# Kernel optimization log

Measured on AMD Instinct MI355X. Metric: run time of the kernel, lower is better.

The kernel has to match this reference:

```python
import jax, jax.numpy as jnp
import numpy as np

DG = 4      # deformable groups
PAD = 1     # (kernel_size - 1) // 2
KH = KW = 3


def deform_conv(x, offset, weight, dg=DG, pad=PAD):
    """DCN v1 (mmcv layout): offset channels = dg * 2 * K, per group ordered
    (y0, x0, y1, x1, ...) over kernel points in row-major order.
    x: [B, C, H, W]; offset: [B, dg*2*K, H, W]; weight: [Cout, C, kh, kw].
    """
    B, C, H, W = x.shape
    Cout, Cin, kh, kw = weight.shape
    K = kh * kw
    Cg = C // dg
    off = offset.reshape(B, dg, K, 2, H, W)

    ys = jnp.arange(H, dtype=x.dtype)
    xs = jnp.arange(W, dtype=x.dtype)
    kyy = jnp.repeat(jnp.arange(kh, dtype=x.dtype) - pad, kw)   # [K]
    kxx = jnp.tile(jnp.arange(kw, dtype=x.dtype) - pad, kh)     # [K]

    # fractional sampling positions, [B, dg, K, H, W]
    py = ys[None, :, None] + kyy[:, None, None] + off[:, :, :, 0]
    px = xs[None, None, :] + kxx[:, None, None] + off[:, :, :, 1]

    y0 = jnp.floor(py)
    x0 = jnp.floor(px)
    ty = py - y0
    tx = px - x0
    y1 = y0 + 1.0
    x1 = x0 + 1.0

    x_flat = x.reshape(B, dg, Cg, H * W)
    acc = jnp.zeros((B, dg, Cg, K, H, W), dtype=x.dtype)
    corners = [
        (y0, x0, (1.0 - ty) * (1.0 - tx)),
        (y0, x1, (1.0 - ty) * tx),
        (y1, x0, ty * (1.0 - tx)),
        (y1, x1, ty * tx),
    ]
    for yc, xc, wgt in corners:
        valid = (yc >= 0) & (yc <= H - 1) & (xc >= 0) & (xc <= W - 1)
        yi = jnp.clip(yc, 0, H - 1).astype(jnp.int32)
        xi = jnp.clip(xc, 0, W - 1).astype(jnp.int32)
        idx = (yi * W + xi).reshape(B, dg, 1, K * H * W)
        v = jnp.take_along_axis(x_flat, idx, axis=3).reshape(B, dg, Cg, K, H, W)
        wv = jnp.where(valid, wgt, 0.0)[:, :, None]  # [B, dg, 1, K, H, W]
        acc = acc + v * wv

    w = weight.reshape(Cout, dg, Cg, kh * kw)
    return jnp.einsum('bgckhw,ogck->bohw', acc, w)


def setup_inputs() -> dict:
    key = jax.random.key(0)
    ks = jax.random.split(key, 6)
    B, C, H, W = 8, 256, 64, 64
    return {
        'reg_feat': jax.random.normal(ks[0], (B, C, H, W), jnp.float32),
        'cls_feat': jax.random.normal(ks[1], (B, C, H, W), jnp.float32),
        'pred_init': jax.random.normal(ks[2], (B, 34, H, W), jnp.float32),
        'w_offset': jax.random.normal(ks[3], (DG * 2 * KH * KW, 34), jnp.float32) * 0.1,
        'w_reg': jax.random.normal(ks[4], (C, C, KH, KW), jnp.float32) * 0.01,
        'w_cls': jax.random.normal(ks[5], (C, C, KH, KW), jnp.float32) * 0.01,
    }


def reference(reg_feat, cls_feat, pred_init, w_offset, w_reg, w_cls):
    # 1x1 offset conv on detached anchor-shape prediction
    offset = jnp.einsum('bchw,oc->bohw', jax.lax.stop_gradient(pred_init), w_offset)
    reg_refine = jax.nn.relu(deform_conv(reg_feat, offset, w_reg))
    cls_refine = jax.nn.relu(deform_conv(cls_feat, offset, w_cls))
    return (reg_refine, cls_refine)
```

## Files before the change

### kernel.cpp

```cpp
#include <hip/hip_runtime.h>

#define B_   8
#define C_   256
#define HW_  4096
#define OC_  72
#define PC_  34
#define CLS_OFF (B_ * C_ * HW_)

typedef __attribute__((ext_vector_type(8))) short short8v;
typedef __attribute__((ext_vector_type(4))) float f32x4;

__device__ __forceinline__ ushort f2bf(float f) {
  uint u = __float_as_uint(f);
  return (ushort)((u + 0x7fffu + ((u >> 16) & 1u)) >> 16);
}
__device__ __forceinline__ float bf2f(ushort h) {
  return __uint_as_float(((uint)h) << 16);
}

__global__ __launch_bounds__(256)
void offset_kernel(const float* __restrict__ pred, const float* __restrict__ wo,
                   float* __restrict__ offset) {
  const int p  = blockIdx.x * 256 + threadIdx.x;
  const int b  = p >> 12;
  const int hw = p & 4095;
  const float* pp = pred + (size_t)b * PC_ * HW_ + hw;
  float v[PC_];
#pragma unroll
  for (int i = 0; i < PC_; ++i) v[i] = pp[(size_t)i * HW_];
  float* op = offset + (size_t)b * OC_ * HW_ + hw;
  for (int o = 0; o < OC_; ++o) {
    float s = 0.f;
#pragma unroll
    for (int i = 0; i < PC_; ++i) s = fmaf(v[i], wo[o * PC_ + i], s);
    op[(size_t)o * HW_] = s;
  }
}

__global__ __launch_bounds__(256)
void repack_w(const float* __restrict__ w_reg, const float* __restrict__ w_cls,
              ushort* __restrict__ wpk) {
  const int tid = blockIdx.x * 256 + threadIdx.x;
  const int l   = tid & 63;
  const int mf  = (tid >> 6) & 15;
  int rest = tid >> 10;
  const int kk  = rest & 1; rest >>= 1;
  const int s   = rest % 36;
  const int map = rest / 36;
  const float* src = map ? w_cls : w_reg;
  const int g = s / 9, kp = s % 9;
  const int o = mf * 16 + (l & 15);
  const int cbase = kk * 32 + (l >> 4) * 8;
  union { ushort u[8]; short8v v; } hu, lu;
#pragma unroll
  for (int j = 0; j < 8; ++j) {
    const int c = cbase + j;
    const float v = src[o * 2304 + (g * 64 + c) * 9 + kp];
    const ushort h = f2bf(v);
    hu.u[j] = h;
    lu.u[j] = f2bf(v - bf2f(h));
  }
  const size_t eb = ((size_t)((map * 36 + s) * 2 + kk)) * 16384 + mf * 512 + l * 8;
  *reinterpret_cast<short8v*>(wpk + eb)        = hu.v;
  *reinterpret_cast<short8v*>(wpk + eb + 8192) = lu.v;
}

__device__ __forceinline__ void calc_params(const float* __restrict__ off, int b,
                                            int px0, int t, int ss,
                                            int (*sIdx)[64][4], float (*sWt)[64][4],
                                            int bb) {
  const int hw = px0 + t;
  const int y = hw >> 6, x = hw & 63;
  const int kp = ss % 9;
  const float oy = off[((size_t)b * OC_ + 2 * ss) * HW_ + hw];
  const float ox = off[((size_t)b * OC_ + 2 * ss + 1) * HW_ + hw];
  const float py  = (float)(y + kp / 3 - 1) + oy;
  const float pxx = (float)(x + kp % 3 - 1) + ox;
  const float y0f = floorf(py), x0f = floorf(pxx);
  const float ty = py - y0f, tx = pxx - x0f;
  const int y0 = (int)y0f, x0 = (int)x0f;
  const int y1 = y0 + 1, x1 = x0 + 1;
  const bool vy0 = (y0 >= 0) & (y0 <= 63), vy1 = (y1 >= 0) & (y1 <= 63);
  const bool vx0 = (x0 >= 0) & (x0 <= 63), vx1 = (x1 >= 0) & (x1 <= 63);
  const int cy0 = min(max(y0, 0), 63), cy1 = min(max(y1, 0), 63);
  const int cx0 = min(max(x0, 0), 63), cx1 = min(max(x1, 0), 63);
  sIdx[bb][t][0] = cy0 * 64 + cx0; sWt[bb][t][0] = (vy0 && vx0) ? (1.f - ty) * (1.f - tx) : 0.f;
  sIdx[bb][t][1] = cy0 * 64 + cx1; sWt[bb][t][1] = (vy0 && vx1) ? (1.f - ty) * tx : 0.f;
  sIdx[bb][t][2] = cy1 * 64 + cx0; sWt[bb][t][2] = (vy1 && vx0) ? ty * (1.f - tx) : 0.f;
  sIdx[bb][t][3] = cy1 * 64 + cx1; sWt[bb][t][3] = (vy1 && vx1) ? ty * tx : 0.f;
}

__global__ __launch_bounds__(256)
void deform_mfma(const float* __restrict__ xreg, const float* __restrict__ xcls,
                 const float* __restrict__ off, const ushort* __restrict__ wpk,
                 float* __restrict__ out) {
  __shared__ ushort Bh[4096];
  __shared__ ushort Bl[4096];
  __shared__ int   sIdx[2][64][4];
  __shared__ float sWt[2][64][4];

  const int lin = blockIdx.y * 512 + blockIdx.x;
  const int nid = (lin & 7) * 128 + (lin >> 3);
  const int map = nid >> 9;
  const int nt  = nid & 511;
  const int b   = nt >> 6;
  const int px0 = (nt & 63) * 64;

  const int t = threadIdx.x;
  const int lane = t & 63, wid = t >> 6;
  const float* xsrc = map ? xcls : xreg;

  f32x4 acc[4][4];
#pragma unroll
  for (int mf = 0; mf < 4; ++mf)
#pragma unroll
    for (int nf = 0; nf < 4; ++nf) acc[mf][nf] = (f32x4){0.f, 0.f, 0.f, 0.f};

  if (t < 64) calc_params(off, b, px0, t, 0, sIdx, sWt, 0);
  __syncthreads();

  for (int s = 0; s < 36; ++s) {
    const int pb = s & 1;
    const int g  = s / 9;

    short8v a_h[2][4], a_l[2][4];
    const size_t abase = ((size_t)(map * 36 + s)) * 32768 + lane * 8;
#pragma unroll
    for (int kk = 0; kk < 2; ++kk)
#pragma unroll
      for (int mf = 0; mf < 4; ++mf) {
        const size_t e = abase + (size_t)kk * 16384 + (wid * 4 + mf) * 512;
        a_h[kk][mf] = *reinterpret_cast<const short8v*>(wpk + e);
        a_l[kk][mf] = *reinterpret_cast<const short8v*>(wpk + e + 8192);
      }

    {
      const int px  = t & 63;
      const int kgb = t >> 6;
      const int i0 = sIdx[pb][px][0], i1 = sIdx[pb][px][1],
                i2 = sIdx[pb][px][2], i3 = sIdx[pb][px][3];
      const float w0 = sWt[pb][px][0], w1 = sWt[pb][px][1],
                  w2 = sWt[pb][px][2], w3 = sWt[pb][px][3];
#pragma unroll
      for (int q = 0; q < 2; ++q) {
        const int kg = kgb + q * 4;
        const float* xb = xsrc + ((size_t)((b * 4 + g) * 64 + kg * 8)) * HW_;
        union { ushort u[8]; short8v v; } hu, lu;
#pragma unroll
        for (int i = 0; i < 8; ++i) {
          const float* xc = xb + (size_t)i * HW_;
          const float v = w0 * xc[i0] + w1 * xc[i1] + w2 * xc[i2] + w3 * xc[i3];
          const ushort h = f2bf(v);
          hu.u[i] = h;
          lu.u[i] = f2bf(v - bf2f(h));
        }
        const int slot = ((kg >> 2) * 4 + (px >> 4)) * 64 + ((kg & 3) * 16 + (px & 15));
        *reinterpret_cast<short8v*>(Bh + slot * 8) = hu.v;
        *reinterpret_cast<short8v*>(Bl + slot * 8) = lu.v;
      }
    }

    if (s + 1 < 36 && t < 64) calc_params(off, b, px0, t, s + 1, sIdx, sWt, pb ^ 1);
    __syncthreads();

#pragma unroll
    for (int kk = 0; kk < 2; ++kk) {
      short8v bh[4], bl[4];
#pragma unroll
      for (int nf = 0; nf < 4; ++nf) {
        bh[nf] = *reinterpret_cast<const short8v*>(Bh + ((kk * 4 + nf) * 64 + lane) * 8);
        bl[nf] = *reinterpret_cast<const short8v*>(Bl + ((kk * 4 + nf) * 64 + lane) * 8);
      }
#pragma unroll
      for (int mf = 0; mf < 4; ++mf)
#pragma unroll
        for (int nf = 0; nf < 4; ++nf) {
          f32x4 c = acc[mf][nf];
          c = __builtin_amdgcn_mfma_f32_16x16x32_bf16(a_l[kk][mf], bh[nf], c, 0, 0, 0);
          c = __builtin_amdgcn_mfma_f32_16x16x32_bf16(a_h[kk][mf], bl[nf], c, 0, 0, 0);
          c = __builtin_amdgcn_mfma_f32_16x16x32_bf16(a_h[kk][mf], bh[nf], c, 0, 0, 0);
          acc[mf][nf] = c;
        }
    }
    __syncthreads();
  }

  float* obase = out + (map ? CLS_OFF : 0) + (size_t)b * C_ * HW_ + px0;
  const int m0 = wid * 64;
#pragma unroll
  for (int mf = 0; mf < 4; ++mf)
#pragma unroll
    for (int nf = 0; nf < 4; ++nf)
#pragma unroll
      for (int r = 0; r < 4; ++r) {
        const int o = m0 + mf * 16 + (lane >> 4) * 4 + r;
        const int n = nf * 16 + (lane & 15);
        obase[(size_t)o * HW_ + n] = fmaxf(acc[mf][nf][r], 0.f);
      }
}

extern "C" void kernel_launch(void* const* d_in, const int* in_sizes, int n_in,
                              void* d_out, int out_size, void* d_ws, size_t ws_size,
                              hipStream_t stream) {
  const float* reg_feat = (const float*)d_in[0];
  const float* cls_feat = (const float*)d_in[1];
  const float* pred     = (const float*)d_in[2];
  const float* w_off    = (const float*)d_in[3];
  const float* w_reg    = (const float*)d_in[4];
  const float* w_cls    = (const float*)d_in[5];
  float* outp = (float*)d_out;

  float*  offset = (float*)d_ws;
  ushort* wpk    = (ushort*)((char*)d_ws + (size_t)B_ * OC_ * HW_ * 4);

  offset_kernel<<<dim3((B_ * HW_) / 256), 256, 0, stream>>>(pred, w_off, offset);
  repack_w<<<dim3(576), 256, 0, stream>>>(w_reg, w_cls, wpk);
  deform_mfma<<<dim3(512, 2), dim3(256), 0, stream>>>(reg_feat, cls_feat,
                                                      offset, wpk, outp);
}
```

Before: 637.5 us.

## Software-pipeline deformable gather with MFMA using double-buffered LDS and merged prep kernel

The main kernel now double-buffers the bf16 hi/lo B tiles in LDS. It issues the global gathers for step s+1 into registers before running the MFMAs for step s, then converts and stores them afterwards, so gather latency overlaps with matrix math and one barrier per step is removed. Bilinear parameters are computed per thread in registers from prefetched offsets instead of being staged through shared memory. The offset and weight-repack kernels are merged into one launch, and launch bounds, s_setprio and a changed LDS slot mapping are added. The cost is higher register pressure (64 gathered floats per thread), which may limit occupancy.

```diff
diff --git a/kernel.cpp b/kernel.cpp
--- a/kernel.cpp
+++ b/kernel.cpp
@@ -19,63 +19,57 @@
 }
 
 __global__ __launch_bounds__(256)
-void offset_kernel(const float* __restrict__ pred, const float* __restrict__ wo,
-                   float* __restrict__ offset) {
-  const int p  = blockIdx.x * 256 + threadIdx.x;
-  const int b  = p >> 12;
-  const int hw = p & 4095;
-  const float* pp = pred + (size_t)b * PC_ * HW_ + hw;
-  float v[PC_];
-#pragma unroll
-  for (int i = 0; i < PC_; ++i) v[i] = pp[(size_t)i * HW_];
-  float* op = offset + (size_t)b * OC_ * HW_ + hw;
-  for (int o = 0; o < OC_; ++o) {
-    float s = 0.f;
-#pragma unroll
-    for (int i = 0; i < PC_; ++i) s = fmaf(v[i], wo[o * PC_ + i], s);
-    op[(size_t)o * HW_] = s;
+void prep_kernel(const float* __restrict__ pred, const float* __restrict__ wo,
+                 const float* __restrict__ w_reg, const float* __restrict__ w_cls,
+                 float* __restrict__ offset, ushort* __restrict__ wpk) {
+  if (blockIdx.x < 128) {
+    const int p  = blockIdx.x * 256 + threadIdx.x;
+    const int b  = p >> 12;
+    const int hw = p & 4095;
+    const float* pp = pred + (size_t)b * PC_ * HW_ + hw;
+    float v[PC_];
+#pragma unroll
+    for (int i = 0; i < PC_; ++i) v[i] = pp[(size_t)i * HW_];
+    float* op = offset + (size_t)b * OC_ * HW_ + hw;
+    for (int o = 0; o < OC_; ++o) {
+      float s = 0.f;
+#pragma unroll
+      for (int i = 0; i < PC_; ++i) s = fmaf(v[i], wo[o * PC_ + i], s);
+      op[(size_t)o * HW_] = s;
+    }
+  } else {
+    const int tid = (blockIdx.x - 128) * 256 + threadIdx.x;
+    const int l   = tid & 63;
+    const int mf  = (tid >> 6) & 15;
+    int rest = tid >> 10;
+    const int kk  = rest & 1; rest >>= 1;
+    const int s   = rest % 36;
+    const int map = rest / 36;
+    const float* src = map ? w_cls : w_reg;
+    const int g = s / 9, kp = s % 9;
+    const int o = mf * 16 + (l & 15);
+    const int cbase = kk * 32 + (l >> 4) * 8;
+    union { ushort u[8]; short8v v; } hu, lu;
+#pragma unroll
+    for (int j = 0; j < 8; ++j) {
+      const int c = cbase + j;
+      const float v = src[o * 2304 + (g * 64 + c) * 9 + kp];
+      const ushort h = f2bf(v);
+      hu.u[j] = h;
+      lu.u[j] = f2bf(v - bf2f(h));
+    }
+    const size_t eb = ((size_t)((map * 36 + s) * 2 + kk)) * 16384 + mf * 512 + l * 8;
+    *reinterpret_cast<short8v*>(wpk + eb)        = hu.v;
+    *reinterpret_cast<short8v*>(wpk + eb + 8192) = lu.v;
   }
 }
 
-__global__ __launch_bounds__(256)
-void repack_w(const float* __restrict__ w_reg, const float* __restrict__ w_cls,
-              ushort* __restrict__ wpk) {
-  const int tid = blockIdx.x * 256 + threadIdx.x;
-  const int l   = tid & 63;
-  const int mf  = (tid >> 6) & 15;
-  int rest = tid >> 10;
-  const int kk  = rest & 1; rest >>= 1;
-  const int s   = rest % 36;
-  const int map = rest / 36;
-  const float* src = map ? w_cls : w_reg;
-  const int g = s / 9, kp = s % 9;
-  const int o = mf * 16 + (l & 15);
-  const int cbase = kk * 32 + (l >> 4) * 8;
-  union { ushort u[8]; short8v v; } hu, lu;
-#pragma unroll
-  for (int j = 0; j < 8; ++j) {
-    const int c = cbase + j;
-    const float v = src[o * 2304 + (g * 64 + c) * 9 + kp];
-    const ushort h = f2bf(v);
-    hu.u[j] = h;
-    lu.u[j] = f2bf(v - bf2f(h));
-  }
-  const size_t eb = ((size_t)((map * 36 + s) * 2 + kk)) * 16384 + mf * 512 + l * 8;
-  *reinterpret_cast<short8v*>(wpk + eb)        = hu.v;
-  *reinterpret_cast<short8v*>(wpk + eb + 8192) = lu.v;
-}
-
-__device__ __forceinline__ void calc_params(const float* __restrict__ off, int b,
-                                            int px0, int t, int ss,
-                                            int (*sIdx)[64][4], float (*sWt)[64][4],
-                                            int bb) {
-  const int hw = px0 + t;
-  const int y = hw >> 6, x = hw & 63;
+__device__ __forceinline__ void calcp(float oy, float ox, int ss, int yy, int xx,
+                                      int& i0, int& i1, int& i2, int& i3,
+                                      float& w0, float& w1, float& w2, float& w3) {
   const int kp = ss % 9;
-  const float oy = off[((size_t)b * OC_ + 2 * ss) * HW_ + hw];
-  const float ox = off[((size_t)b * OC_ + 2 * ss + 1) * HW_ + hw];
-  const float py  = (float)(y + kp / 3 - 1) + oy;
-  const float pxx = (float)(x + kp % 3 - 1) + ox;
+  const float py  = (float)(yy + kp / 3 - 1) + oy;
+  const float pxx = (float)(xx + kp % 3 - 1) + ox;
   const float y0f = floorf(py), x0f = floorf(pxx);
   const float ty = py - y0f, tx = pxx - x0f;
   const int y0 = (int)y0f, x0 = (int)x0f;
@@ -84,30 +78,31 @@
   const bool vx0 = (x0 >= 0) & (x0 <= 63), vx1 = (x1 >= 0) & (x1 <= 63);
   const int cy0 = min(max(y0, 0), 63), cy1 = min(max(y1, 0), 63);
   const int cx0 = min(max(x0, 0), 63), cx1 = min(max(x1, 0), 63);
-  sIdx[bb][t][0] = cy0 * 64 + cx0; sWt[bb][t][0] = (vy0 && vx0) ? (1.f - ty) * (1.f - tx) : 0.f;
-  sIdx[bb][t][1] = cy0 * 64 + cx1; sWt[bb][t][1] = (vy0 && vx1) ? (1.f - ty) * tx : 0.f;
-  sIdx[bb][t][2] = cy1 * 64 + cx0; sWt[bb][t][2] = (vy1 && vx0) ? ty * (1.f - tx) : 0.f;
-  sIdx[bb][t][3] = cy1 * 64 + cx1; sWt[bb][t][3] = (vy1 && vx1) ? ty * tx : 0.f;
-}
-
-__global__ __launch_bounds__(256)
+  i0 = cy0 * 64 + cx0;  w0 = (vy0 && vx0) ? (1.f - ty) * (1.f - tx) : 0.f;
+  i1 = cy0 * 64 + cx1;  w1 = (vy0 && vx1) ? (1.f - ty) * tx         : 0.f;
+  i2 = cy1 * 64 + cx0;  w2 = (vy1 && vx0) ? ty * (1.f - tx)         : 0.f;
+  i3 = cy1 * 64 + cx1;  w3 = (vy1 && vx1) ? ty * tx                 : 0.f;
+}
+
+__global__ __launch_bounds__(256, 2)
 void deform_mfma(const float* __restrict__ xreg, const float* __restrict__ xcls,
                  const float* __restrict__ off, const ushort* __restrict__ wpk,
                  float* __restrict__ out) {
-  __shared__ ushort Bh[4096];
-  __shared__ ushort Bl[4096];
-  __shared__ int   sIdx[2][64][4];
-  __shared__ float sWt[2][64][4];
+  __shared__ ushort Bh[2][4096];
+  __shared__ ushort Bl[2][4096];
 
   const int lin = blockIdx.y * 512 + blockIdx.x;
   const int nid = (lin & 7) * 128 + (lin >> 3);
   const int map = nid >> 9;
   const int nt  = nid & 511;
   const int b   = nt >> 6;
-  const int px0 = (nt & 63) * 64;
+  const int yy  = nt & 63;
+  const int px0 = yy * 64;
 
   const int t = threadIdx.x;
   const int lane = t & 63, wid = t >> 6;
+  const int px = t & 63;
+  const int kgb = wid;
   const float* xsrc = map ? xcls : xreg;
 
   f32x4 acc[4][4];
@@ -116,71 +111,109 @@
 #pragma unroll
     for (int nf = 0; nf < 4; ++nf) acc[mf][nf] = (f32x4){0.f, 0.f, 0.f, 0.f};
 
-  if (t < 64) calc_params(off, b, px0, t, 0, sIdx, sWt, 0);
+  const size_t obidx = ((size_t)b * OC_) * HW_ + px0 + px;
+  float offY = off[obidx];
+  float offX = off[obidx + HW_];
+
+  {
+    int i0, i1, i2, i3; float w0, w1, w2, w3;
+    calcp(offY, offX, 0, yy, px, i0, i1, i2, i3, w0, w1, w2, w3);
+    const float* xb = xsrc + ((size_t)(b * 4 * 64 + kgb * 8)) * HW_;
+    float rc0[16], rc1[16], rc2[16], rc3[16];
+#pragma unroll
+    for (int q = 0; q < 2; ++q)
+#pragma unroll
+      for (int i = 0; i < 8; ++i) {
+        const float* xc = xb + (size_t)(q * 32 + i) * HW_;
+        rc0[q * 8 + i] = xc[i0]; rc1[q * 8 + i] = xc[i1];
+        rc2[q * 8 + i] = xc[i2]; rc3[q * 8 + i] = xc[i3];
+      }
+    offY = off[obidx + 2 * HW_];
+    offX = off[obidx + 3 * HW_];
+#pragma unroll
+    for (int q = 0; q < 2; ++q) {
+      union { ushort u[8]; short8v v; } hu, lu;
+#pragma unroll
+      for (int i = 0; i < 8; ++i) {
+        const float v = w0 * rc0[q * 8 + i] + w1 * rc1[q * 8 + i]
+                      + w2 * rc2[q * 8 + i] + w3 * rc3[q * 8 + i];
+        const ushort h = f2bf(v);
+        hu.u[i] = h; lu.u[i] = f2bf(v - bf2f(h));
+      }
+      const int slot = (q * 4 + (px >> 4)) * 64 + kgb * 16 + (px & 15);
+      *reinterpret_cast<short8v*>(&Bh[0][slot * 8]) = hu.v;
+      *reinterpret_cast<short8v*>(&Bl[0][slot * 8]) = lu.v;
+    }
+  }
   __syncthreads();
 
   for (int s = 0; s < 36; ++s) {
-    const int pb = s & 1;
-    const int g  = s / 9;
+    const int cb = s & 1, nb = cb ^ 1;
 
     short8v a_h[2][4], a_l[2][4];
-    const size_t abase = ((size_t)(map * 36 + s)) * 32768 + lane * 8;
+    const size_t abase = ((size_t)(map * 36 + s)) * 32768 + (size_t)lane * 8;
 #pragma unroll
     for (int kk = 0; kk < 2; ++kk)
 #pragma unroll
       for (int mf = 0; mf < 4; ++mf) {
-        const size_t e = abase + (size_t)kk * 16384 + (wid * 4 + mf) * 512;
+        const size_t e = abase + (size_t)kk * 16384 + (size_t)(wid * 4 + mf) * 512;
         a_h[kk][mf] = *reinterpret_cast<const short8v*>(wpk + e);
         a_l[kk][mf] = *reinterpret_cast<const short8v*>(wpk + e + 8192);
       }
 
-    {
-      const int px  = t & 63;
-      const int kgb = t >> 6;
-      const int i0 = sIdx[pb][px][0], i1 = sIdx[pb][px][1],
-                i2 = sIdx[pb][px][2], i3 = sIdx[pb][px][3];
-      const float w0 = sWt[pb][px][0], w1 = sWt[pb][px][1],
-                  w2 = sWt[pb][px][2], w3 = sWt[pb][px][3];
-#pragma unroll
-      for (int q = 0; q < 2; ++q) {
-        const int kg = kgb + q * 4;
-        const float* xb = xsrc + ((size_t)((b * 4 + g) * 64 + kg * 8)) * HW_;
-        union { ushort u[8]; short8v v; } hu, lu;
+    int i0, i1, i2, i3; float w0, w1, w2, w3;
+    float rc0[16], rc1[16], rc2[16], rc3[16];
+    if (s < 35) {
+      calcp(offY, offX, s + 1, yy, px, i0, i1, i2, i3, w0, w1, w2, w3);
+      const int g1 = (s + 1) / 9;
+      const float* xb = xsrc + ((size_t)((b * 4 + g1) * 64 + kgb * 8)) * HW_;
+#pragma unroll
+      for (int q = 0; q < 2; ++q)
 #pragma unroll
         for (int i = 0; i < 8; ++i) {
-          const float* xc = xb + (size_t)i * HW_;
-          const float v = w0 * xc[i0] + w1 * xc[i1] + w2 * xc[i2] + w3 * xc[i3];
-          const ushort h = f2bf(v);
-          hu.u[i] = h;
-          lu.u[i] = f2bf(v - bf2f(h));
+          const float* xc = xb + (size_t)(q * 32 + i) * HW_;
+          rc0[q * 8 + i] = xc[i0]; rc1[q * 8 + i] = xc[i1];
+          rc2[q * 8 + i] = xc[i2]; rc3[q * 8 + i] = xc[i3];
         }
-        const int slot = ((kg >> 2) * 4 + (px >> 4)) * 64 + ((kg & 3) * 16 + (px & 15));
-        *reinterpret_cast<short8v*>(Bh + slot * 8) = hu.v;
-        *reinterpret_cast<short8v*>(Bl + slot * 8) = lu.v;
-      }
-    }
-
-    if (s + 1 < 36 && t < 64) calc_params(off, b, px0, t, s + 1, sIdx, sWt, pb ^ 1);
-    __syncthreads();
-
-#pragma unroll
-    for (int kk = 0; kk < 2; ++kk) {
-      short8v bh[4], bl[4];
+      if (s < 34) {
+        offY = off[obidx + (size_t)(2 * s + 4) * HW_];
+        offX = off[obidx + (size_t)(2 * s + 5) * HW_];
+      }
+    }
+
+    __builtin_amdgcn_s_setprio(1);
+#pragma unroll
+    for (int kk = 0; kk < 2; ++kk)
 #pragma unroll
       for (int nf = 0; nf < 4; ++nf) {
-        bh[nf] = *reinterpret_cast<const short8v*>(Bh + ((kk * 4 + nf) * 64 + lane) * 8);
-        bl[nf] = *reinterpret_cast<const short8v*>(Bl + ((kk * 4 + nf) * 64 + lane) * 8);
-      }
-#pragma unroll
-      for (int mf = 0; mf < 4; ++mf)
-#pragma unroll
-        for (int nf = 0; nf < 4; ++nf) {
+        const short8v bh = *reinterpret_cast<const short8v*>(&Bh[cb][((kk * 4 + nf) * 64 + lane) * 8]);
+        const short8v bl = *reinterpret_cast<const short8v*>(&Bl[cb][((kk * 4 + nf) * 64 + lane) * 8]);
+#pragma unroll
+        for (int mf = 0; mf < 4; ++mf) {
           f32x4 c = acc[mf][nf];
-          c = __builtin_amdgcn_mfma_f32_16x16x32_bf16(a_l[kk][mf], bh[nf], c, 0, 0, 0);
-          c = __builtin_amdgcn_mfma_f32_16x16x32_bf16(a_h[kk][mf], bl[nf], c, 0, 0, 0);
-          c = __builtin_amdgcn_mfma_f32_16x16x32_bf16(a_h[kk][mf], bh[nf], c, 0, 0, 0);
+          c = __builtin_amdgcn_mfma_f32_16x16x32_bf16(a_l[kk][mf], bh, c, 0, 0, 0);
+          c = __builtin_amdgcn_mfma_f32_16x16x32_bf16(a_h[kk][mf], bl, c, 0, 0, 0);
+          c = __builtin_amdgcn_mfma_f32_16x16x32_bf16(a_h[kk][mf], bh, c, 0, 0, 0);
           acc[mf][nf] = c;
         }
+      }
+    __builtin_amdgcn_s_setprio(0);
+
+    if (s < 35) {
+#pragma unroll
+      for (int q = 0; q < 2; ++q) {
+        union { ushort u[8]; short8v v; } hu, lu;
+#pragma unroll
+        for (int i = 0; i < 8; ++i) {
+          const float v = w0 * rc0[q * 8 + i] + w1 * rc1[q * 8 + i]
+                        + w2 * rc2[q * 8 + i] + w3 * rc3[q * 8 + i];
+          const ushort h = f2bf(v);
+          hu.u[i] = h; lu.u[i] = f2bf(v - bf2f(h));
+        }
+        const int slot = (q * 4 + (px >> 4)) * 64 + kgb * 16 + (px & 15);
+        *reinterpret_cast<short8v*>(&Bh[nb][slot * 8]) = hu.v;
+        *reinterpret_cast<short8v*>(&Bl[nb][slot * 8]) = lu.v;
+      }
     }
     __syncthreads();
   }
@@ -213,8 +246,8 @@
   float*  offset = (float*)d_ws;
   ushort* wpk    = (ushort*)((char*)d_ws + (size_t)B_ * OC_ * HW_ * 4);
 
-  offset_kernel<<<dim3((B_ * HW_) / 256), 256, 0, stream>>>(pred, w_off, offset);
-  repack_w<<<dim3(576), 256, 0, stream>>>(w_reg, w_cls, wpk);
+  prep_kernel<<<dim3(704), 256, 0, stream>>>(pred, w_off, w_reg, w_cls,
+                                             offset, wpk);
   deform_mfma<<<dim3(512, 2), dim3(256), 0, stream>>>(reg_feat, cls_feat,
                                                       offset, wpk, outp);
 }
```

After: 623.1 us. 1.02x faster.
